# Optimization experiments

Measured on AMD Instinct MI355X. Metric: run time of the kernel, lower is better.

Reference implementation:

```python
import math
import jax, jax.numpy as jnp
import numpy as np

B, N, CS, CZ, H, C, PQ, PV = 1, 1024, 384, 128, 12, 16, 4, 8
INF = 1e5
EPS = 1e-8
COUT = H * (CZ + C + PV * 4)  # 2112


def setup_inputs() -> dict:
    key = jax.random.key(0)
    ks = jax.random.split(key, 16)
    scale = 0.02
    s = jax.random.normal(ks[0], (B, N, CS), jnp.float32)
    z = jax.random.normal(ks[1], (B, N, N, CZ), jnp.float32)
    rot, _ = jnp.linalg.qr(jax.random.normal(ks[2], (B, N, 3, 3), jnp.float32))
    trans = jax.random.normal(ks[3], (B, N, 3), jnp.float32)
    mask = jnp.ones((B, N), jnp.float32)
    hc = H * C
    Wq = jax.random.normal(ks[4], (hc, CS), jnp.float32) * scale
    bq = jnp.zeros((hc,), jnp.float32)
    Wkv = jax.random.normal(ks[5], (2 * hc, CS), jnp.float32) * scale
    bkv = jnp.zeros((2 * hc,), jnp.float32)
    Wqp = jax.random.normal(ks[6], (H * PQ * 3, CS), jnp.float32) * scale
    bqp = jnp.zeros((H * PQ * 3,), jnp.float32)
    Wkvp = jax.random.normal(ks[7], (H * (PQ + PV) * 3, CS), jnp.float32) * scale
    bkvp = jnp.zeros((H * (PQ + PV) * 3,), jnp.float32)
    Wb = jax.random.normal(ks[8], (H, CZ), jnp.float32) * scale
    bb = jnp.zeros((H,), jnp.float32)
    # softplus^{-1}(1) init, as in ipa_point_weights_init_
    head_weights = jnp.full((H,), float(np.log(np.e - 1.0)), jnp.float32)
    Wout = jax.random.normal(ks[9], (CS, COUT), jnp.float32) * scale
    bout = jnp.zeros((CS,), jnp.float32)
    return dict(s=s, z=z, rot=rot, trans=trans, mask=mask, Wq=Wq, bq=bq,
                Wkv=Wkv, bkv=bkv, Wqp=Wqp, bqp=bqp, Wkvp=Wkvp, bkvp=bkvp,
                Wb=Wb, bb=bb, head_weights=head_weights, Wout=Wout, bout=bout)


def _ipa(s, z, rot, trans, mask, Wq, bq, Wkv, bkv, Wqp, bqp, Wkvp, bkvp,
         Wb, bb, head_weights, Wout, bout):
    # scalar q, k, v: [B,N,H,C]
    q = (s @ Wq.T + bq).reshape(B, N, H, C)
    kv = (s @ Wkv.T + bkv).reshape(B, N, H, 2 * C)
    k, v = kv[..., :C], kv[..., C:]

    def proj_points(W, b, P):
        pl = s @ W.T + b                                    # [B,N,H*P*3]
        pts = jnp.stack(jnp.split(pl, 3, axis=-1), axis=-1)  # [B,N,H*P,3]
        g = jnp.einsum('bnij,bnpj->bnpi', rot, pts) + trans[:, :, None, :]
        return g.reshape(B, N, H, P, 3)

    q_pts = proj_points(Wqp, bqp, PQ)                  # [B,N,H,PQ,3]
    kv_pts = proj_points(Wkvp, bkvp, PQ + PV)          # [B,N,H,PQ+PV,3]
    k_pts, v_pts = kv_pts[..., :PQ, :], kv_pts[..., PQ:, :]

    b_bias = z @ Wb.T + bb                             # [B,N,N,H]
    a = jnp.einsum('bihc,bjhc->bhij', q, k) * math.sqrt(1.0 / (3 * C))
    a = a + math.sqrt(1.0 / 3) * jnp.transpose(b_bias, (0, 3, 1, 2))

    # squared point distances [B,i,j,H,PQ]
    d2 = jnp.sum((q_pts[:, :, None] - k_pts[:, None]) ** 2, axis=-1)
    hw = jax.nn.softplus(head_weights) * math.sqrt(1.0 / (3 * (PQ * 9.0 / 2)))
    pt = -0.5 * jnp.sum(d2 * hw[None, None, None, :, None], axis=-1)  # [B,i,j,H]
    a = a + jnp.transpose(pt, (0, 3, 1, 2))

    sq_mask = INF * (mask[:, :, None] * mask[:, None, :] - 1.0)
    a = jax.nn.softmax(a + sq_mask[:, None], axis=-1)  # [B,H,i,j]

    o = jnp.einsum('bhij,bjhc->bihc', a, v).reshape(B, N, H * C)
    o_pt = jnp.einsum('bhij,bjhpx->bihpx', a, v_pts)   # [B,N,H,PV,3] global
    o_pt = jnp.einsum('bnji,bnhpj->bnhpi', rot, o_pt - trans[:, :, None, None, :])
    o_pt_norm = jnp.sqrt(jnp.sum(o_pt ** 2, axis=-1) + EPS).reshape(B, N, H * PV)
    o_pt = o_pt.reshape(B, N, H * PV, 3)
    o_pair = jnp.einsum('bhij,bijc->bihc', a, z).reshape(B, N, H * CZ)

    cat = jnp.concatenate(
        [o, o_pt[..., 0], o_pt[..., 1], o_pt[..., 2], o_pt_norm, o_pair], axis=-1)
    return cat @ Wout.T + bout


def reference(s, z, rot, trans, mask, Wq, bq, Wkv, bkv, Wqp, bqp, Wkvp, bkvp,
              Wb, bb, head_weights, Wout, bout):
    return _ipa(s, z, rot, trans, mask, Wq, bq, Wkv, bkv, Wqp, bqp, Wkvp, bkvp,
                Wb, bb, head_weights, Wout, bout)
```

## Files before the change

kernel.cpp:

```cpp
#include <hip/hip_runtime.h>
#include <hip/hip_bf16.h>
#include <math.h>

#define NN   1024
#define CSD  384
#define CZD  128
#define HD   12
#define NOUT 1152
#define COUTD 2112

__device__ __forceinline__ float4 ld4(const float* p) {
    return *reinterpret_cast<const float4*>(p);
}

__global__ __launch_bounds__(384) void k_proj(
    const float* __restrict__ s,
    const float* __restrict__ Wq,   const float* __restrict__ bq,
    const float* __restrict__ Wkv,  const float* __restrict__ bkv,
    const float* __restrict__ Wqp,  const float* __restrict__ bqp,
    const float* __restrict__ Wkvp, const float* __restrict__ bkvp,
    float* __restrict__ pl)
{
    __shared__ float s_lds[16 * CSD];
    const int rb = blockIdx.x * 16;
    const int t  = threadIdx.x;
    for (int e = t; e < 16 * CSD; e += 384) s_lds[e] = s[(size_t)rb * CSD + e];
    __syncthreads();
    const int o = blockIdx.y * 384 + t;
    const float* W; float bias;
    if (o < 192)      { W = Wq   + (size_t)o * CSD;        bias = bq[o]; }
    else if (o < 576) { W = Wkv  + (size_t)(o-192) * CSD;  bias = bkv[o-192]; }
    else if (o < 720) { W = Wqp  + (size_t)(o-576) * CSD;  bias = bqp[o-576]; }
    else              { W = Wkvp + (size_t)(o-720) * CSD;  bias = bkvp[o-720]; }
    float acc[16];
    #pragma unroll
    for (int r = 0; r < 16; ++r) acc[r] = bias;
    for (int k = 0; k < CSD; k += 4) {
        float4 w4 = ld4(W + k);
        #pragma unroll
        for (int r = 0; r < 16; ++r) {
            float4 s4 = ld4(&s_lds[r * CSD + k]);
            acc[r] += w4.x*s4.x + w4.y*s4.y + w4.z*s4.z + w4.w*s4.w;
        }
    }
    #pragma unroll
    for (int r = 0; r < 16; ++r) pl[(size_t)(rb + r) * NOUT + o] = acc[r];
}

__global__ __launch_bounds__(384) void k_scatter(
    const float* __restrict__ pl, const float* __restrict__ rot,
    const float* __restrict__ trans,
    float* __restrict__ qrec, float* __restrict__ krec, float* __restrict__ vrec)
{
    const int n = blockIdx.x, t = threadIdx.x;
    __shared__ float R[9], T[3];
    if (t < 9)  R[t] = rot[n*9 + t];
    if (t >= 9 && t < 12) T[t-9] = trans[n*3 + t - 9];
    __syncthreads();
    const float s48 = 0.14433756729740643f;
    const float* p = pl + (size_t)n * NOUT;
    for (int u = t; u < 768; u += 384) {
        if (u < 192) {
            int h = u >> 4, c = u & 15;
            qrec[((size_t)n*HD + h)*28 + c] = p[u] * s48;
        } else if (u < 576) {
            int e = u - 192, h = e >> 5, ee = e & 31;
            float val = p[u];
            if (ee < 16) krec[((size_t)n*HD + h)*28 + ee]      = val;
            else         vrec[((size_t)n*HD + h)*40 + (ee-16)] = val;
        } else if (u < 624) {
            int hp = u - 576;
            float x = p[576 + hp], y = p[576 + 48 + hp], zz = p[576 + 96 + hp];
            float gx = R[0]*x + R[1]*y + R[2]*zz + T[0];
            float gy = R[3]*x + R[4]*y + R[5]*zz + T[1];
            float gz = R[6]*x + R[7]*y + R[8]*zz + T[2];
            int h = hp >> 2, pp = hp & 3;
            float* d = qrec + ((size_t)n*HD + h)*28 + 16 + pp*3;
            d[0] = gx; d[1] = gy; d[2] = gz;
        } else {
            int hp = u - 624;
            float x = p[720 + hp], y = p[720 + 144 + hp], zz = p[720 + 288 + hp];
            float gx = R[0]*x + R[1]*y + R[2]*zz + T[0];
            float gy = R[3]*x + R[4]*y + R[5]*zz + T[1];
            float gz = R[6]*x + R[7]*y + R[8]*zz + T[2];
            int h = hp / 12, pp = hp % 12;
            if (pp < 4) {
                float* d = krec + ((size_t)n*HD + h)*28 + 16 + pp*3;
                d[0] = gx; d[1] = gy; d[2] = gz;
            } else {
                float* d = vrec + ((size_t)n*HD + h)*40 + 16 + (pp-4)*3;
                d[0] = gx; d[1] = gy; d[2] = gz;
            }
        }
    }
}

__global__ __launch_bounds__(256) void k_logits(
    const float* __restrict__ z, const float* __restrict__ qrec,
    const float* __restrict__ krec, const float* __restrict__ Wb,
    const float* __restrict__ bb, const float* __restrict__ hwin,
    const float* __restrict__ mask, float* __restrict__ L)
{
    const int i  = blockIdx.x;
    const int j0 = blockIdx.y * 64;
    const int t  = threadIdx.x;
    __shared__ float wbs[HD * CZD];
    __shared__ float qr[HD * 28];
    __shared__ float bbs[HD], hws[HD];
    const float s3 = 0.5773502691896258f;
    for (int e = t; e < HD * CZD; e += 256) wbs[e] = Wb[e] * s3;
    for (int e = t; e < HD * 28;  e += 256) qr[e]  = qrec[(size_t)i*HD*28 + e];
    if (t < HD) {
        bbs[t] = bb[t] * s3;
        float x = hwin[t];
        hws[t] = -0.5f * log1pf(expf(x)) * 0.13608276348795434f;
    }
    __syncthreads();
    const int jj = t & 63;
    const int g  = t >> 6;
    const int j  = j0 + jj;
    const float* zrow = z + ((size_t)i * NN + j) * CZD;
    float acc0 = bbs[3*g+0], acc1 = bbs[3*g+1], acc2 = bbs[3*g+2];
    for (int c = 0; c < CZD; c += 4) {
        float4 zv = ld4(zrow + c);
        float4 w0 = ld4(&wbs[(3*g+0)*CZD + c]);
        float4 w1 = ld4(&wbs[(3*g+1)*CZD + c]);
        float4 w2 = ld4(&wbs[(3*g+2)*CZD + c]);
        acc0 += zv.x*w0.x + zv.y*w0.y + zv.z*w0.z + zv.w*w0.w;
        acc1 += zv.x*w1.x + zv.y*w1.y + zv.z*w1.z + zv.w*w1.w;
        acc2 += zv.x*w2.x + zv.y*w2.y + zv.z*w2.z + zv.w*w2.w;
    }
    const float mterm = 100000.0f * (mask[i] * mask[j] - 1.0f);
    float biases[3] = {acc0, acc1, acc2};
    #pragma unroll
    for (int r = 0; r < 3; ++r) {
        const int h = 3*g + r;
        const float* kr = krec + ((size_t)j*HD + h)*28;
        const float* q  = qr + h*28;
        float qk = 0.f, d2 = 0.f;
        #pragma unroll
        for (int c = 0; c < 16; ++c) qk += q[c] * kr[c];
        #pragma unroll
        for (int e = 0; e < 12; ++e) { float d = q[16+e] - kr[16+e]; d2 += d*d; }
        L[((size_t)i*HD + h)*NN + j] = biases[r] + qk + hws[h]*d2 + mterm;
    }
}

__global__ __launch_bounds__(384) void k_accum(
    const float* __restrict__ z, const float* __restrict__ L,
    const float* __restrict__ vrec,
    float* __restrict__ cat, float* __restrict__ optg)
{
    const int i = blockIdx.x, t = threadIdx.x;
    __shared__ float Ls[HD * NN];
    __shared__ float l_s[HD];
    for (int e = t; e < HD*NN/4; e += 384)
        reinterpret_cast<float4*>(Ls)[e] =
            reinterpret_cast<const float4*>(L + (size_t)i*HD*NN)[e];
    __syncthreads();
    const int lane = t & 63, wv = t >> 6;
    for (int hh = 0; hh < 2; ++hh) {
        const int h = wv*2 + hh;
        float mx = -1e30f;
        for (int k = lane; k < NN; k += 64) mx = fmaxf(mx, Ls[h*NN + k]);
        #pragma unroll
        for (int d = 32; d; d >>= 1) mx = fmaxf(mx, __shfl_xor(mx, d));
        float sum = 0.f;
        for (int k = lane; k < NN; k += 64) {
            float pe = __expf(Ls[h*NN + k] - mx);
            Ls[h*NN + k] = pe;
            sum += pe;
        }
        #pragma unroll
        for (int d = 32; d; d >>= 1) sum += __shfl_xor(sum, d);
        if (lane == 0) l_s[h] = sum;
    }
    __syncthreads();
    const int h = t >> 5, cq = t & 31;
    const float inv_l = 1.0f / l_s[h];
    float ax=0.f, ay=0.f, az=0.f, aw=0.f, a0=0.f, a1=0.f;
    const float* zr0 = z + (size_t)i * NN * CZD;
    for (int jj = 0; jj < NN; jj += 4) {
        const float4 p4 = ld4(&Ls[h*NN + jj]);
        #pragma unroll
        for (int u = 0; u < 4; ++u) {
            const float p = (u==0)?p4.x:(u==1)?p4.y:(u==2)?p4.z:p4.w;
            const float4 zv = ld4(zr0 + (size_t)(jj+u)*CZD + cq*4);
            ax += p*zv.x; ay += p*zv.y; az += p*zv.z; aw += p*zv.w;
            const float* v = vrec + ((size_t)(jj+u)*HD + h)*40;
            a0 += p * v[cq];
            float vb = (cq < 8) ? v[32 + cq] : 0.f;
            a1 += p * vb;
        }
    }
    float* cc = cat + (size_t)i * COUTD;
    float4 op; op.x = ax*inv_l; op.y = ay*inv_l; op.z = az*inv_l; op.w = aw*inv_l;
    *reinterpret_cast<float4*>(cc + 576 + h*128 + cq*4) = op;
    a0 *= inv_l; a1 *= inv_l;
    if (cq < 16) cc[h*16 + cq] = a0;
    else optg[((size_t)i*HD + h)*24 + (cq - 16)] = a0;
    if (cq < 8)  optg[((size_t)i*HD + h)*24 + 16 + cq] = a1;
}

__global__ __launch_bounds__(128) void k_optrot(
    const float* __restrict__ optg, const float* __restrict__ rot,
    const float* __restrict__ trans, float* __restrict__ cat)
{
    const int n = blockIdx.x, t = threadIdx.x;
    __shared__ float R[9], T[3];
    if (t < 9)  R[t] = rot[n*9 + t];
    if (t >= 9 && t < 12) T[t-9] = trans[n*3 + t-9];
    __syncthreads();
    if (t < 96) {
        const float* g = optg + (size_t)n*HD*24 + t*3;
        float x = g[0]-T[0], y = g[1]-T[1], zz = g[2]-T[2];
        float lx = R[0]*x + R[3]*y + R[6]*zz;
        float ly = R[1]*x + R[4]*y + R[7]*zz;
        float lz = R[2]*x + R[5]*y + R[8]*zz;
        float nrm = sqrtf(lx*lx + ly*ly + lz*lz + 1e-8f);
        float* cc = cat + (size_t)n * COUTD;
        cc[192 + t] = lx;
        cc[288 + t] = ly;
        cc[384 + t] = lz;
        cc[480 + t] = nrm;
    }
}

__global__ __launch_bounds__(192) void k_out(
    const float* __restrict__ cat, const float* __restrict__ Wout,
    const float* __restrict__ bout, float* __restrict__ out)
{
    const int rb = blockIdx.x * 16;
    const int cb = blockIdx.y * 96;
    const int t  = threadIdx.x;
    const int c2 = t % 48;
    const int rg = t / 48;
    const int c  = cb + c2*2;
    __shared__ float cs[16 * 64];
    float acc[4][2] = {};
    const float* w0 = Wout + (size_t)c * COUTD;
    const float* w1 = w0 + COUTD;
    for (int k0 = 0; k0 < COUTD; k0 += 64) {
        __syncthreads();
        for (int e = t; e < 256; e += 192) {
            int row = e >> 4, c4 = (e & 15) * 4;
            *reinterpret_cast<float4*>(&cs[row*64 + c4]) =
                ld4(cat + (size_t)(rb+row)*COUTD + k0 + c4);
        }
        __syncthreads();
        for (int kk = 0; kk < 64; kk += 4) {
            float4 a = ld4(w0 + k0 + kk);
            float4 b = ld4(w1 + k0 + kk);
            #pragma unroll
            for (int r = 0; r < 4; ++r) {
                float4 cv = ld4(&cs[(rg*4+r)*64 + kk]);
                acc[r][0] += cv.x*a.x + cv.y*a.y + cv.z*a.z + cv.w*a.w;
                acc[r][1] += cv.x*b.x + cv.y*b.y + cv.z*b.z + cv.w*b.w;
            }
        }
    }
    #pragma unroll
    for (int r = 0; r < 4; ++r) {
        out[(size_t)(rb + rg*4 + r)*CSD + c]     = acc[r][0] + bout[c];
        out[(size_t)(rb + rg*4 + r)*CSD + c + 1] = acc[r][1] + bout[c+1];
    }
}

extern "C" void kernel_launch(void* const* d_in, const int* in_sizes, int n_in,
                              void* d_out, int out_size, void* d_ws, size_t ws_size,
                              hipStream_t stream)
{
    const float* s     = (const float*)d_in[0];
    const float* z     = (const float*)d_in[1];
    const float* rot   = (const float*)d_in[2];
    const float* trans = (const float*)d_in[3];
    const float* mask  = (const float*)d_in[4];
    const float* Wq    = (const float*)d_in[5];
    const float* bq    = (const float*)d_in[6];
    const float* Wkv   = (const float*)d_in[7];
    const float* bkv   = (const float*)d_in[8];
    const float* Wqp   = (const float*)d_in[9];
    const float* bqp   = (const float*)d_in[10];
    const float* Wkvp  = (const float*)d_in[11];
    const float* bkvp  = (const float*)d_in[12];
    const float* Wb    = (const float*)d_in[13];
    const float* bb    = (const float*)d_in[14];
    const float* hw    = (const float*)d_in[15];
    const float* Wout  = (const float*)d_in[16];
    const float* bout  = (const float*)d_in[17];
    float* out = (float*)d_out;

    float* w    = (float*)d_ws;
    float* pl   = w;
    float* qrec = pl   + (size_t)NN * NOUT;
    float* krec = qrec + (size_t)NN * HD * 28;
    float* vrec = krec + (size_t)NN * HD * 28;
    float* L    = vrec + (size_t)NN * HD * 40;
    float* cat  = L    + (size_t)NN * HD * NN;
    float* optg = cat  + (size_t)NN * COUTD;

    k_proj   <<<dim3(64, 3),  dim3(384), 0, stream>>>(s, Wq, bq, Wkv, bkv, Wqp, bqp, Wkvp, bkvp, pl);
    k_scatter<<<dim3(NN),     dim3(384), 0, stream>>>(pl, rot, trans, qrec, krec, vrec);
    k_logits <<<dim3(NN, 16), dim3(256), 0, stream>>>(z, qrec, krec, Wb, bb, hw, mask, L);
    k_accum  <<<dim3(NN),     dim3(384), 0, stream>>>(z, L, vrec, cat, optg);
    k_optrot <<<dim3(NN),     dim3(128), 0, stream>>>(optg, rot, trans, cat);
    k_out    <<<dim3(64, 4),  dim3(192), 0, stream>>>(cat, Wout, bout, out);
}
```

Baseline: 1.638 ms.

## Fuse logits and accumulation into flash-style online-softmax kernel reading z once

Merges the logits kernel and the accumulation kernel into one kernel that streams 64-row tiles of z into shared memory. Each tile is used both for the pair bias and for the weighted z sum, with an online softmax carrying the running max and sum. This removes the second full read of z (512MB) and the write and read of the logits buffer. The point-distance term is expanded algebraically into a dot product with folded per-key constants, so the query-key step becomes one 32-wide dot product. The cost is extra barriers per tile and a grid of only 1024 blocks for the z-heavy work.

```diff
diff --git a/kernel.cpp b/kernel.cpp
--- a/kernel.cpp
+++ b/kernel.cpp
@@ -47,156 +47,166 @@
     for (int r = 0; r < 16; ++r) pl[(size_t)(rb + r) * NOUT + o] = acc[r];
 }
 
-__global__ __launch_bounds__(384) void k_scatter(
+__global__ __launch_bounds__(192) void k_scatter(
     const float* __restrict__ pl, const float* __restrict__ rot,
-    const float* __restrict__ trans,
-    float* __restrict__ qrec, float* __restrict__ krec, float* __restrict__ vrec)
+    const float* __restrict__ trans, const float* __restrict__ hwin,
+    const float* __restrict__ bb,
+    float* __restrict__ qa, float* __restrict__ ka, float* __restrict__ vrec)
 {
     const int n = blockIdx.x, t = threadIdx.x;
+    const int h = t >> 4, e = t & 15;
     __shared__ float R[9], T[3];
+    __shared__ float kp2p[48];
     if (t < 9)  R[t] = rot[n*9 + t];
     if (t >= 9 && t < 12) T[t-9] = trans[n*3 + t - 9];
     __syncthreads();
     const float s48 = 0.14433756729740643f;
+    const float s3  = 0.5773502691896258f;
+    const float sp  = log1pf(expf(hwin[h]));
+    const float hws = -0.5f * sp * 0.13608276348795434f;
     const float* p = pl + (size_t)n * NOUT;
-    for (int u = t; u < 768; u += 384) {
-        if (u < 192) {
-            int h = u >> 4, c = u & 15;
-            qrec[((size_t)n*HD + h)*28 + c] = p[u] * s48;
-        } else if (u < 576) {
-            int e = u - 192, h = e >> 5, ee = e & 31;
-            float val = p[u];
-            if (ee < 16) krec[((size_t)n*HD + h)*28 + ee]      = val;
-            else         vrec[((size_t)n*HD + h)*40 + (ee-16)] = val;
-        } else if (u < 624) {
-            int hp = u - 576;
-            float x = p[576 + hp], y = p[576 + 48 + hp], zz = p[576 + 96 + hp];
-            float gx = R[0]*x + R[1]*y + R[2]*zz + T[0];
-            float gy = R[3]*x + R[4]*y + R[5]*zz + T[1];
-            float gz = R[6]*x + R[7]*y + R[8]*zz + T[2];
-            int h = hp >> 2, pp = hp & 3;
-            float* d = qrec + ((size_t)n*HD + h)*28 + 16 + pp*3;
-            d[0] = gx; d[1] = gy; d[2] = gz;
+    float* qan = qa   + ((size_t)n*HD + h)*32;
+    float* kan = ka   + ((size_t)n*HD + h)*32;
+    float* vn  = vrec + ((size_t)n*HD + h)*40;
+    qan[e] = p[h*16 + e] * s48;
+    kan[e] = p[192 + h*32 + e];
+    vn[e]  = p[192 + h*32 + 16 + e];
+    if (e < 12) {
+        float x = p[720 + h*12 + e], y = p[720 + 144 + h*12 + e], zz = p[720 + 288 + h*12 + e];
+        float gx = R[0]*x + R[1]*y + R[2]*zz + T[0];
+        float gy = R[3]*x + R[4]*y + R[5]*zz + T[1];
+        float gz = R[6]*x + R[7]*y + R[8]*zz + T[2];
+        if (e < 4) {
+            kan[16 + 3*e] = gx; kan[16 + 3*e + 1] = gy; kan[16 + 3*e + 2] = gz;
+            kp2p[h*4 + e] = gx*gx + gy*gy + gz*gz;
         } else {
-            int hp = u - 624;
-            float x = p[720 + hp], y = p[720 + 144 + hp], zz = p[720 + 288 + hp];
-            float gx = R[0]*x + R[1]*y + R[2]*zz + T[0];
-            float gy = R[3]*x + R[4]*y + R[5]*zz + T[1];
-            float gz = R[6]*x + R[7]*y + R[8]*zz + T[2];
-            int h = hp / 12, pp = hp % 12;
-            if (pp < 4) {
-                float* d = krec + ((size_t)n*HD + h)*28 + 16 + pp*3;
-                d[0] = gx; d[1] = gy; d[2] = gz;
-            } else {
-                float* d = vrec + ((size_t)n*HD + h)*40 + 16 + (pp-4)*3;
-                d[0] = gx; d[1] = gy; d[2] = gz;
+            vn[16 + 3*(e-4)] = gx; vn[16 + 3*(e-4) + 1] = gy; vn[16 + 3*(e-4) + 2] = gz;
+        }
+    } else {
+        int pp = e - 12;
+        float x = p[576 + h*4 + pp], y = p[576 + 48 + h*4 + pp], zz = p[576 + 96 + h*4 + pp];
+        float gx = R[0]*x + R[1]*y + R[2]*zz + T[0];
+        float gy = R[3]*x + R[4]*y + R[5]*zz + T[1];
+        float gz = R[6]*x + R[7]*y + R[8]*zz + T[2];
+        float c = -2.0f * hws;
+        qan[16 + 3*pp] = gx*c; qan[16 + 3*pp + 1] = gy*c; qan[16 + 3*pp + 2] = gz*c;
+    }
+    __syncthreads();
+    if (e == 0) {
+        kan[28] = hws * (kp2p[h*4] + kp2p[h*4+1] + kp2p[h*4+2] + kp2p[h*4+3]) + s3 * bb[h];
+        kan[29] = 0.f; kan[30] = 0.f; kan[31] = 0.f;
+        qan[28] = 1.f; qan[29] = 0.f; qan[30] = 0.f; qan[31] = 0.f;
+    }
+}
+
+__global__ __launch_bounds__(384) void k_attn(
+    const float* __restrict__ z,   const float* __restrict__ qa,
+    const float* __restrict__ ka,  const float* __restrict__ vrec,
+    const float* __restrict__ Wb,  const float* __restrict__ mask,
+    float* __restrict__ cat, float* __restrict__ optg)
+{
+    const int i = blockIdx.x, t = threadIdx.x;
+    __shared__ float4 zt4[64 * 32];
+    __shared__ float  wbs[HD * CZD];
+    __shared__ float  qas[HD * 32];
+    __shared__ float  st[HD * 64];
+    __shared__ float  ptile[HD * 64];
+    __shared__ float  mS[HD], lS[HD], aS[HD];
+
+    const float s3 = 0.5773502691896258f;
+    for (int e = t; e < HD * CZD; e += 384) wbs[e] = Wb[e] * s3;
+    for (int e = t; e < HD * 32;  e += 384) qas[e] = qa[(size_t)i*HD*32 + e];
+    if (t < HD) { mS[t] = -1e30f; lS[t] = 0.f; }
+    const float mi = mask[i];
+
+    const int h  = t >> 5, cq = t & 31;
+    float ax=0.f, ay=0.f, az=0.f, aw=0.f, a0=0.f, a1=0.f;
+
+    const int jj = t & 63, g = t >> 6;
+    const int lane = t & 63, wv = t >> 6;
+
+    const float* zbase = z + (size_t)i * NN * CZD;
+
+    for (int j0 = 0; j0 < NN; j0 += 64) {
+        __syncthreads();
+        for (int e = t; e < 64 * 32; e += 384) {
+            int row = e >> 5, s = e & 31;
+            float4 v4 = ld4(zbase + (size_t)(j0 + row) * CZD + s * 4);
+            zt4[row * 32 + (s ^ (row & 31))] = v4;
+        }
+        __syncthreads();
+        {
+            const int h0 = 2*g, h1 = 2*g + 1;
+            float b0 = 0.f, b1 = 0.f;
+            const int rbase = jj * 32, rx = jj & 31;
+            #pragma unroll 8
+            for (int s = 0; s < 32; ++s) {
+                float4 zv = zt4[rbase + (s ^ rx)];
+                float4 w0 = ld4(&wbs[h0 * CZD + 4*s]);
+                float4 w1 = ld4(&wbs[h1 * CZD + 4*s]);
+                b0 += zv.x*w0.x + zv.y*w0.y + zv.z*w0.z + zv.w*w0.w;
+                b1 += zv.x*w1.x + zv.y*w1.y + zv.z*w1.z + zv.w*w1.w;
             }
-        }
-    }
-}
-
-__global__ __launch_bounds__(256) void k_logits(
-    const float* __restrict__ z, const float* __restrict__ qrec,
-    const float* __restrict__ krec, const float* __restrict__ Wb,
-    const float* __restrict__ bb, const float* __restrict__ hwin,
-    const float* __restrict__ mask, float* __restrict__ L)
-{
-    const int i  = blockIdx.x;
-    const int j0 = blockIdx.y * 64;
-    const int t  = threadIdx.x;
-    __shared__ float wbs[HD * CZD];
-    __shared__ float qr[HD * 28];
-    __shared__ float bbs[HD], hws[HD];
-    const float s3 = 0.5773502691896258f;
-    for (int e = t; e < HD * CZD; e += 256) wbs[e] = Wb[e] * s3;
-    for (int e = t; e < HD * 28;  e += 256) qr[e]  = qrec[(size_t)i*HD*28 + e];
-    if (t < HD) {
-        bbs[t] = bb[t] * s3;
-        float x = hwin[t];
-        hws[t] = -0.5f * log1pf(expf(x)) * 0.13608276348795434f;
-    }
-    __syncthreads();
-    const int jj = t & 63;
-    const int g  = t >> 6;
-    const int j  = j0 + jj;
-    const float* zrow = z + ((size_t)i * NN + j) * CZD;
-    float acc0 = bbs[3*g+0], acc1 = bbs[3*g+1], acc2 = bbs[3*g+2];
-    for (int c = 0; c < CZD; c += 4) {
-        float4 zv = ld4(zrow + c);
-        float4 w0 = ld4(&wbs[(3*g+0)*CZD + c]);
-        float4 w1 = ld4(&wbs[(3*g+1)*CZD + c]);
-        float4 w2 = ld4(&wbs[(3*g+2)*CZD + c]);
-        acc0 += zv.x*w0.x + zv.y*w0.y + zv.z*w0.z + zv.w*w0.w;
-        acc1 += zv.x*w1.x + zv.y*w1.y + zv.z*w1.z + zv.w*w1.w;
-        acc2 += zv.x*w2.x + zv.y*w2.y + zv.z*w2.z + zv.w*w2.w;
-    }
-    const float mterm = 100000.0f * (mask[i] * mask[j] - 1.0f);
-    float biases[3] = {acc0, acc1, acc2};
-    #pragma unroll
-    for (int r = 0; r < 3; ++r) {
-        const int h = 3*g + r;
-        const float* kr = krec + ((size_t)j*HD + h)*28;
-        const float* q  = qr + h*28;
-        float qk = 0.f, d2 = 0.f;
+            const int j = j0 + jj;
+            const float* ka0 = ka + ((size_t)j*HD + h0)*32;
+            const float* ka1 = ka + ((size_t)j*HD + h1)*32;
+            float q0 = 0.f, q1 = 0.f;
+            #pragma unroll
+            for (int s = 0; s < 8; ++s) {
+                float4 k0 = ld4(ka0 + 4*s);
+                float4 k1 = ld4(ka1 + 4*s);
+                float4 a0v = ld4(&qas[h0*32 + 4*s]);
+                float4 a1v = ld4(&qas[h1*32 + 4*s]);
+                q0 += k0.x*a0v.x + k0.y*a0v.y + k0.z*a0v.z + k0.w*a0v.w;
+                q1 += k1.x*a1v.x + k1.y*a1v.y + k1.z*a1v.z + k1.w*a1v.w;
+            }
+            const float mterm = 100000.0f * (mi * mask[j] - 1.0f);
+            st[h0*64 + jj] = b0 + q0 + mterm;
+            st[h1*64 + jj] = b1 + q1 + mterm;
+        }
+        __syncthreads();
         #pragma unroll
-        for (int c = 0; c < 16; ++c) qk += q[c] * kr[c];
-        #pragma unroll
-        for (int e = 0; e < 12; ++e) { float d = q[16+e] - kr[16+e]; d2 += d*d; }
-        L[((size_t)i*HD + h)*NN + j] = biases[r] + qk + hws[h]*d2 + mterm;
-    }
-}
-
-__global__ __launch_bounds__(384) void k_accum(
-    const float* __restrict__ z, const float* __restrict__ L,
-    const float* __restrict__ vrec,
-    float* __restrict__ cat, float* __restrict__ optg)
-{
-    const int i = blockIdx.x, t = threadIdx.x;
-    __shared__ float Ls[HD * NN];
-    __shared__ float l_s[HD];
-    for (int e = t; e < HD*NN/4; e += 384)
-        reinterpret_cast<float4*>(Ls)[e] =
-            reinterpret_cast<const float4*>(L + (size_t)i*HD*NN)[e];
-    __syncthreads();
-    const int lane = t & 63, wv = t >> 6;
-    for (int hh = 0; hh < 2; ++hh) {
-        const int h = wv*2 + hh;
-        float mx = -1e30f;
-        for (int k = lane; k < NN; k += 64) mx = fmaxf(mx, Ls[h*NN + k]);
-        #pragma unroll
-        for (int d = 32; d; d >>= 1) mx = fmaxf(mx, __shfl_xor(mx, d));
-        float sum = 0.f;
-        for (int k = lane; k < NN; k += 64) {
-            float pe = __expf(Ls[h*NN + k] - mx);
-            Ls[h*NN + k] = pe;
-            sum += pe;
-        }
-        #pragma unroll
-        for (int d = 32; d; d >>= 1) sum += __shfl_xor(sum, d);
-        if (lane == 0) l_s[h] = sum;
-    }
-    __syncthreads();
-    const int h = t >> 5, cq = t & 31;
-    const float inv_l = 1.0f / l_s[h];
-    float ax=0.f, ay=0.f, az=0.f, aw=0.f, a0=0.f, a1=0.f;
-    const float* zr0 = z + (size_t)i * NN * CZD;
-    for (int jj = 0; jj < NN; jj += 4) {
-        const float4 p4 = ld4(&Ls[h*NN + jj]);
-        #pragma unroll
-        for (int u = 0; u < 4; ++u) {
-            const float p = (u==0)?p4.x:(u==1)?p4.y:(u==2)?p4.z:p4.w;
-            const float4 zv = ld4(zr0 + (size_t)(jj+u)*CZD + cq*4);
-            ax += p*zv.x; ay += p*zv.y; az += p*zv.z; aw += p*zv.w;
-            const float* v = vrec + ((size_t)(jj+u)*HD + h)*40;
-            a0 += p * v[cq];
-            float vb = (cq < 8) ? v[32 + cq] : 0.f;
-            a1 += p * vb;
-        }
-    }
+        for (int hh = 0; hh < 2; ++hh) {
+            const int hs = 2*wv + hh;
+            float sv = st[hs*64 + lane];
+            float mx = sv;
+            #pragma unroll
+            for (int d = 32; d; d >>= 1) mx = fmaxf(mx, __shfl_xor(mx, d));
+            float mold = mS[hs];
+            float mnew = fmaxf(mold, mx);
+            float al   = __expf(mold - mnew);
+            float pe   = __expf(sv - mnew);
+            ptile[hs*64 + lane] = pe;
+            float sum = pe;
+            #pragma unroll
+            for (int d = 32; d; d >>= 1) sum += __shfl_xor(sum, d);
+            if (lane == 0) { mS[hs] = mnew; lS[hs] = lS[hs]*al + sum; aS[hs] = al; }
+        }
+        __syncthreads();
+        {
+            const float al = aS[h];
+            ax *= al; ay *= al; az *= al; aw *= al; a0 *= al; a1 *= al;
+            for (int u = 0; u < 64; u += 4) {
+                float4 p4 = ld4(&ptile[h*64 + u]);
+                #pragma unroll
+                for (int q = 0; q < 4; ++q) {
+                    const int jr = u + q;
+                    const float pw = (q==0)?p4.x:(q==1)?p4.y:(q==2)?p4.z:p4.w;
+                    float4 zv = zt4[jr * 32 + (cq ^ (jr & 31))];
+                    ax += pw*zv.x; ay += pw*zv.y; az += pw*zv.z; aw += pw*zv.w;
+                    const float* v = vrec + ((size_t)(j0 + jr)*HD + h)*40;
+                    a0 += pw * v[cq];
+                    float vb = (cq < 8) ? v[32 + cq] : 0.f;
+                    a1 += pw * vb;
+                }
+            }
+        }
+    }
+    const float inv = 1.0f / lS[h];
     float* cc = cat + (size_t)i * COUTD;
-    float4 op; op.x = ax*inv_l; op.y = ay*inv_l; op.z = az*inv_l; op.w = aw*inv_l;
+    float4 op; op.x = ax*inv; op.y = ay*inv; op.z = az*inv; op.w = aw*inv;
     *reinterpret_cast<float4*>(cc + 576 + h*128 + cq*4) = op;
-    a0 *= inv_l; a1 *= inv_l;
+    a0 *= inv; a1 *= inv;
     if (cq < 16) cc[h*16 + cq] = a0;
     else optg[((size_t)i*HD + h)*24 + (cq - 16)] = a0;
     if (cq < 8)  optg[((size_t)i*HD + h)*24 + 16 + cq] = a1;
@@ -292,17 +302,15 @@
 
     float* w    = (float*)d_ws;
     float* pl   = w;
-    float* qrec = pl   + (size_t)NN * NOUT;
-    float* krec = qrec + (size_t)NN * HD * 28;
-    float* vrec = krec + (size_t)NN * HD * 28;
-    float* L    = vrec + (size_t)NN * HD * 40;
-    float* cat  = L    + (size_t)NN * HD * NN;
+    float* qa   = pl   + (size_t)NN * NOUT;
+    float* ka   = qa   + (size_t)NN * HD * 32;
+    float* vrec = ka   + (size_t)NN * HD * 32;
+    float* cat  = vrec + (size_t)NN * HD * 40;
     float* optg = cat  + (size_t)NN * COUTD;
 
     k_proj   <<<dim3(64, 3),  dim3(384), 0, stream>>>(s, Wq, bq, Wkv, bkv, Wqp, bqp, Wkvp, bkvp, pl);
-    k_scatter<<<dim3(NN),     dim3(384), 0, stream>>>(pl, rot, trans, qrec, krec, vrec);
-    k_logits <<<dim3(NN, 16), dim3(256), 0, stream>>>(z, qrec, krec, Wb, bb, hw, mask, L);
-    k_accum  <<<dim3(NN),     dim3(384), 0, stream>>>(z, L, vrec, cat, optg);
+    k_scatter<<<dim3(NN),     dim3(192), 0, stream>>>(pl, rot, trans, hw, bb, qa, ka, vrec);
+    k_attn   <<<dim3(NN),     dim3(384), 0, stream>>>(z, qa, ka, vrec, Wb, mask, cat, optg);
     k_optrot <<<dim3(NN),     dim3(128), 0, stream>>>(optg, rot, trans, cat);
     k_out    <<<dim3(64, 4),  dim3(192), 0, stream>>>(cat, Wout, bout, out);
 }
```

Result: faster. 1.593 ms (-2.8%).
